# Optimization experiments

Hardware: AMD Instinct MI355X
Metric: run time of the kernel (lower is better)

The kernel has to match this reference:

```python
import jax, jax.numpy as jnp
import numpy as np

B, S, D, H = 8, 1024, 768, 12
DH = D // H  # 64

def setup_inputs() -> dict:
    key = jax.random.key(0)
    ks = jax.random.split(key, 8)
    return {
        "hidden_states": jax.random.normal(ks[0], (B, S, D), jnp.float32),
        "attention_mask": jnp.zeros((B, 1, 1, S), jnp.float32),
        "click_times": jax.random.uniform(ks[1], (B, S), jnp.float32),
        "Wq": jax.random.normal(ks[2], (D, D), jnp.float32) * 0.02,
        "bq": jnp.zeros((D,), jnp.float32),
        "Wk": jax.random.normal(ks[3], (D, D), jnp.float32) * 0.02,
        "bk": jnp.zeros((D,), jnp.float32),
        "Wv": jax.random.normal(ks[4], (D, D), jnp.float32) * 0.02,
        "bv": jnp.zeros((D,), jnp.float32),
    }

def reference(hidden_states, attention_mask, click_times, Wq, bq, Wk, bk, Wv, bv):
    # Linear projections (torch Linear: x @ W.T + b)
    q = hidden_states @ Wq.T + bq
    k = hidden_states @ Wk.T + bk
    v = hidden_states @ Wv.T + bv
    # [B,S,D] -> [B,H,S,DH]
    def split_heads(x):
        return x.reshape(B, S, H, DH).transpose(0, 2, 1, 3)
    q, k, v = split_heads(q), split_heads(k), split_heads(v)
    scores = jnp.einsum('bhqd,bhkd->bhqk', q, k) / jnp.sqrt(jnp.float32(DH))
    # click_times gate: [B,S] -> [B,1,1,S], multiplicative on scores
    scores = scores * click_times[:, None, None, :]
    scores = scores + attention_mask
    probs = jax.nn.softmax(scores, axis=-1)  # dropout is identity at eval
    ctx = jnp.einsum('bhqk,bhkd->bhqd', probs, v)
    ctx = ctx.transpose(0, 2, 1, 3).reshape(B, S, D)
    return ctx
```

## Files before the change

kernel.cpp:

```cpp
#include <hip/hip_runtime.h>
#include <hip/hip_bf16.h>

#define BB 8
#define SS 1024
#define DD 768
#define HH 12

typedef __attribute__((ext_vector_type(8))) _Float16 f16x8;
typedef __attribute__((ext_vector_type(4))) _Float16 f16x4;
typedef __attribute__((ext_vector_type(4))) float f32x4;

typedef __attribute__((address_space(3))) void lds_void;
typedef const __attribute__((address_space(1))) void gmem_void;
#define GLOAD_LDS16(src, dst) \
    __builtin_amdgcn_global_load_lds((gmem_void*)(src), (lds_void*)(dst), 16, 0, 0)

__global__ void prep_kernel(const float* __restrict__ X,
                            const float* __restrict__ Wq,
                            const float* __restrict__ Wk,
                            const float* __restrict__ Wv,
                            const float* __restrict__ bq,
                            const float* __restrict__ bk,
                            const float* __restrict__ bv,
                            _Float16* __restrict__ Xh,
                            _Float16* __restrict__ Wh,
                            float* __restrict__ bias) {
    const int NX4 = (BB * SS * DD) / 4;
    const int NW4 = (DD * DD) / 4;
    const int tid = blockIdx.x * blockDim.x + threadIdx.x;
    const int nth = gridDim.x * blockDim.x;

    for (int i = tid; i < NX4; i += nth) {
        f32x4 x = ((const f32x4*)X)[i];
        f16x4 h;
        for (int j = 0; j < 4; ++j) h[j] = (_Float16)x[j];
        ((f16x4*)Xh)[i] = h;
    }
    const float* Ws[3] = {Wq, Wk, Wv};
    for (int p = 0; p < 3; ++p) {
        const f32x4* src = (const f32x4*)Ws[p];
        f16x4* dst = (f16x4*)(Wh + (size_t)p * DD * DD);
        for (int i = tid; i < NW4; i += nth) {
            f32x4 x = src[i];
            f16x4 h;
            for (int j = 0; j < 4; ++j) h[j] = (_Float16)x[j];
            dst[i] = h;
        }
    }
    for (int i = tid; i < 3 * DD; i += nth) {
        bias[i] = (i < DD) ? bq[i] : (i < 2 * DD ? bk[i - DD] : bv[i - 2 * DD]);
    }
}

__global__ __launch_bounds__(256, 3) void qkv_gemm(const _Float16* __restrict__ Xh,
                                                   const _Float16* __restrict__ Wh,
                                                   const float* __restrict__ bias,
                                                   _Float16* __restrict__ Qb,
                                                   _Float16* __restrict__ Kb,
                                                   _Float16* __restrict__ Vt) {
    __shared__ __align__(16) _Float16 At[2][128 * 32];
    __shared__ __align__(16) _Float16 Bt[2][128 * 32];

    const int tid = threadIdx.x;
    const int l = tid & 63, w = tid >> 6;
    const int wm = w >> 1, wn = w & 1;
    const int mblk = blockIdx.x * 128, nblk = blockIdx.y * 128;
    const int lr = l & 15, lg = l >> 4;
    const int mbase = mblk + wm * 64, nbase = nblk + wn * 64;

    const int sr_i = l >> 2;
    const int scb  = (l & 3) << 4;
    const int sx   = (sr_i >> 1) & 3;
    const int scol = (scb ^ (sx << 4)) >> 1;

    const _Float16* Ag = Xh + (size_t)(mblk + w * 32 + sr_i) * DD + scol;
    const _Float16* Bg = Wh + (size_t)(nblk + w * 32 + sr_i) * DD + scol;

    const int ax = (lr >> 1) & 3;
    const int acol = (lg ^ ax) << 3;
    const int arow0 = (wm * 64 + lr) * 32 + acol;
    const int brow0 = (wn * 64 + lr) * 32 + acol;

    f32x4 acc[4][4] = {};

#pragma unroll
    for (int i = 0; i < 2; ++i) {
        GLOAD_LDS16(Ag + i * 16 * DD, &At[0][w * 1024 + i * 512]);
        GLOAD_LDS16(Bg + i * 16 * DD, &Bt[0][w * 1024 + i * 512]);
    }
    __syncthreads();

    for (int s_ = 0; s_ < 24; ++s_) {
        const int cur = s_ & 1;
        if (s_ < 23) {
            const int kk = (s_ + 1) * 32;
#pragma unroll
            for (int i = 0; i < 2; ++i) {
                GLOAD_LDS16(Ag + kk + i * 16 * DD, &At[cur ^ 1][w * 1024 + i * 512]);
                GLOAD_LDS16(Bg + kk + i * 16 * DD, &Bt[cur ^ 1][w * 1024 + i * 512]);
            }
        }
        f16x8 a[4], b[4];
#pragma unroll
        for (int mi = 0; mi < 4; ++mi)
            a[mi] = *(const f16x8*)(&At[cur][arow0 + mi * 512]);
#pragma unroll
        for (int ni = 0; ni < 4; ++ni)
            b[ni] = *(const f16x8*)(&Bt[cur][brow0 + ni * 512]);
        __builtin_amdgcn_s_setprio(1);
#pragma unroll
        for (int mi = 0; mi < 4; ++mi)
#pragma unroll
            for (int ni = 0; ni < 4; ++ni)
                acc[mi][ni] = __builtin_amdgcn_mfma_f32_16x16x32_f16(
                    a[mi], b[ni], acc[mi][ni], 0, 0, 0);
        __builtin_amdgcn_s_setprio(0);
        __syncthreads();
    }

#pragma unroll
    for (int ni = 0; ni < 4; ++ni) {
        const int n = nbase + ni * 16 + lr;
        const float bv_ = bias[n];
        const int proj = (n >= 2 * DD) ? 2 : (n >= DD ? 1 : 0);
        const int rem = n - proj * DD;
        const int h = rem >> 6, dh = rem & 63;
#pragma unroll
        for (int mi = 0; mi < 4; ++mi) {
            const int m0 = mbase + mi * 16 + lg * 4;
            const int b_ = m0 >> 10;
            const int s0 = m0 & 1023;
            const int bh = b_ * HH + h;
            f32x4 v = acc[mi][ni];
            if (proj == 2) {
                f16x4 pk;
#pragma unroll
                for (int r = 0; r < 4; ++r) pk[r] = (_Float16)(v[r] + bv_);
                *(f16x4*)(Vt + ((size_t)bh * 64 + dh) * SS + s0) = pk;
            } else {
                _Float16* dst = (proj == 0) ? Qb : Kb;
#pragma unroll
                for (int r = 0; r < 4; ++r)
                    dst[((size_t)bh * SS + (s0 + r)) * 64 + dh] =
                        (_Float16)(v[r] + bv_);
            }
        }
    }
}

__global__ __launch_bounds__(256, 4) void attn_kernel(const _Float16* __restrict__ Qb,
                                                      const _Float16* __restrict__ Kb,
                                                      const _Float16* __restrict__ Vt,
                                                      const float* __restrict__ click,
                                                      const float* __restrict__ mask,
                                                      float* __restrict__ out) {
    __shared__ __align__(16) _Float16 Ksh[2][64 * 64];
    __shared__ __align__(16) _Float16 Vsh[2][64 * 64];
    __shared__ __align__(16) _Float16 pT[4][16][40];

    const int tid = threadIdx.x;
    const int l = tid & 63, w = tid >> 6;
    const int lr = l & 15, lg = l >> 4;
    const int qt = blockIdx.x & 15;
    const int bh = blockIdx.x >> 4;
    const int b_ = bh / HH, h = bh - b_ * HH;
    const int qbase = qt * 64 + w * 16;

    const _Float16* Qp = Qb + (size_t)bh * (SS * 64);
    const _Float16* Kp = Kb + (size_t)bh * (SS * 64);
    const _Float16* Vp = Vt + (size_t)bh * (SS * 64);
    const float* ck = click + b_ * SS;
    const float* mk = mask + b_ * SS;

    const f16x8 qf0 = *(const f16x8*)(Qp + (size_t)(qbase + lr) * 64 + lg * 8);
    const f16x8 qf1 = *(const f16x8*)(Qp + (size_t)(qbase + lr) * 64 + 32 + lg * 8);

    const int srow = l >> 3;
    const int scb  = (l & 7) << 4;
    const int scol = (scb ^ (srow << 4)) >> 1;
    const _Float16* Kg = Kp + (size_t)(w * 16 + srow) * 64 + scol;
    const _Float16* Vg = Vp + (size_t)(w * 16 + srow) * SS + scol;

#pragma unroll
    for (int i = 0; i < 2; ++i) {
        GLOAD_LDS16(Kg + (size_t)(i * 8) * 64, &Ksh[0][w * 1024 + i * 512]);
        GLOAD_LDS16(Vg + (size_t)(i * 8) * SS, &Vsh[0][w * 1024 + i * 512]);
    }
    __syncthreads();

    f32x4 o[4] = {};
    float m_run = -3.0e38f, l_run = 0.f;
    const int sw = (lr & 7) << 4;

    for (int c = 0; c < 16; ++c) {
        const int cur = c & 1;
        if (c < 15) {
            const int nb = (c + 1) * 64;
#pragma unroll
            for (int i = 0; i < 2; ++i) {
                GLOAD_LDS16(Kg + (size_t)(nb + i * 8) * 64, &Ksh[cur ^ 1][w * 1024 + i * 512]);
                GLOAD_LDS16(Vg + nb + (size_t)(i * 8) * SS, &Vsh[cur ^ 1][w * 1024 + i * 512]);
            }
        }
        const _Float16* Ks = Ksh[cur];
        const _Float16* Vs = Vsh[cur];
        const int cb64 = c * 64;

#pragma unroll
        for (int ks = 0; ks < 2; ++ks) {
            f32x4 st[2];
            __builtin_amdgcn_s_setprio(1);
#pragma unroll
            for (int t = 0; t < 2; ++t) {
                const int row = (ks * 2 + t) * 16 + lr;
                const f16x8 kf0 = *(const f16x8*)(Ks + row * 64 + (((lg << 4) ^ sw) >> 1));
                const f16x8 kf1 = *(const f16x8*)(Ks + row * 64 + (((64 | (lg << 4)) ^ sw) >> 1));
                f32x4 z = {};
                z = __builtin_amdgcn_mfma_f32_16x16x32_f16(kf0, qf0, z, 0, 0, 0);
                st[t] = __builtin_amdgcn_mfma_f32_16x16x32_f16(kf1, qf1, z, 0, 0, 0);
            }
            __builtin_amdgcn_s_setprio(0);

            const int koff = cb64 + ks * 32 + lg * 4;
            const f32x4 ck0 = *(const f32x4*)(ck + koff);
            const f32x4 ck1 = *(const f32x4*)(ck + koff + 16);
            const f32x4 mk0 = *(const f32x4*)(mk + koff);
            const f32x4 mk1 = *(const f32x4*)(mk + koff + 16);

            float s0[4], s1[4];
            float tmax = -3.0e38f;
#pragma unroll
            for (int r = 0; r < 4; ++r) {
                s0[r] = st[0][r] * (0.125f * ck0[r]) + mk0[r];
                s1[r] = st[1][r] * (0.125f * ck1[r]) + mk1[r];
                tmax = fmaxf(tmax, fmaxf(s0[r], s1[r]));
            }
            tmax = fmaxf(tmax, __shfl_xor(tmax, 16));
            tmax = fmaxf(tmax, __shfl_xor(tmax, 32));

            if (__any(tmax - m_run > 8.f)) {
                const float m_new = fmaxf(m_run, tmax);
                const float sc = __expf(m_run - m_new);
                l_run *= sc;
#pragma unroll
                for (int f = 0; f < 4; ++f)
#pragma unroll
                    for (int r = 0; r < 4; ++r) o[f][r] *= sc;
                m_run = m_new;
            }

            float psum = 0.f;
            f16x4 pk0, pk1;
#pragma unroll
            for (int r = 0; r < 4; ++r) {
                const float p0 = __expf(s0[r] - m_run);
                const float p1 = __expf(s1[r] - m_run);
                psum += p0 + p1;
                pk0[r] = (_Float16)p0;
                pk1[r] = (_Float16)p1;
            }
            psum += __shfl_xor(psum, 16);
            psum += __shfl_xor(psum, 32);
            l_run += psum;

            *(f16x4*)(&pT[w][lr][lg * 4]) = pk0;
            *(f16x4*)(&pT[w][lr][16 + lg * 4]) = pk1;
            const f16x8 pb = *(const f16x8*)(&pT[w][lr][lg * 8]);

            __builtin_amdgcn_s_setprio(1);
#pragma unroll
            for (int f = 0; f < 4; ++f) {
                const int vrow = f * 16 + lr;
                const f16x8 vf = *(const f16x8*)(Vs + vrow * 64 +
                                                 ((((ks << 6) | (lg << 4)) ^ sw) >> 1));
                o[f] = __builtin_amdgcn_mfma_f32_16x16x32_f16(vf, pb, o[f], 0, 0, 0);
            }
            __builtin_amdgcn_s_setprio(0);
        }
        __syncthreads();
    }

    const float inv = 1.f / l_run;
#pragma unroll
    for (int f = 0; f < 4; ++f) {
        f32x4 v = o[f];
#pragma unroll
        for (int r = 0; r < 4; ++r) v[r] *= inv;
        float* dst = out + ((size_t)(b_ * SS + qbase + lr)) * DD + h * 64 + f * 16 + lg * 4;
        *(f32x4*)dst = v;
    }
}

extern "C" void kernel_launch(void* const* d_in, const int* in_sizes, int n_in,
                              void* d_out, int out_size, void* d_ws, size_t ws_size,
                              hipStream_t stream) {
    const float* X     = (const float*)d_in[0];
    const float* mask  = (const float*)d_in[1];
    const float* click = (const float*)d_in[2];
    const float* Wq    = (const float*)d_in[3];
    const float* bq    = (const float*)d_in[4];
    const float* Wk    = (const float*)d_in[5];
    const float* bk    = (const float*)d_in[6];
    const float* Wv    = (const float*)d_in[7];
    const float* bv    = (const float*)d_in[8];
    float* out = (float*)d_out;

    char* ws = (char*)d_ws;
    _Float16* Xh  = (_Float16*)(ws);
    _Float16* Wh  = (_Float16*)(ws + 12582912);
    float*    bia = (float*)   (ws + 16121856);
    _Float16* Qb  = (_Float16*)(ws + 16131072);
    _Float16* Kb  = (_Float16*)(ws + 28713984);
    _Float16* Vt  = (_Float16*)(ws + 41296896);

    prep_kernel<<<1024, 256, 0, stream>>>(X, Wq, Wk, Wv, bq, bk, bv, Xh, Wh, bia);
    qkv_gemm<<<dim3(64, 18), 256, 0, stream>>>(Xh, Wh, bia, Qb, Kb, Vt);
    attn_kernel<<<BB * HH * (SS / 64), 256, 0, stream>>>(Qb, Kb, Vt, click, mask, out);
}
```

Measured before the change: 208.1 us.

## Process two query tiles per attention wave and remap block IDs for XCD locality

The attention kernel now has each wave handle two 16-row query tiles (128 queries per block), so every K/V fragment read from LDS feeds twice as many MFMAs and the grid is halved. Both the GEMM and attention kernels remap block IDs so that consecutive blocks sharing data land on the same XCD. The click scale is precomputed with the 1/8 factor folded in, the weight conversion loop is flattened, the prep grid is doubled, and the launch bounds are swapped. The cost is higher register pressure in attention, fewer blocks to fill the GPU, and slightly different softmax arithmetic ordering.

```diff
diff --git a/kernel.cpp b/kernel.cpp
--- a/kernel.cpp
+++ b/kernel.cpp
@@ -22,9 +22,11 @@
                             const float* __restrict__ bq,
                             const float* __restrict__ bk,
                             const float* __restrict__ bv,
+                            const float* __restrict__ click,
                             _Float16* __restrict__ Xh,
                             _Float16* __restrict__ Wh,
-                            float* __restrict__ bias) {
+                            float* __restrict__ bias,
+                            float* __restrict__ ckS) {
     const int NX4 = (BB * SS * DD) / 4;
     const int NW4 = (DD * DD) / 4;
     const int tid = blockIdx.x * blockDim.x + threadIdx.x;
@@ -36,23 +38,23 @@
         for (int j = 0; j < 4; ++j) h[j] = (_Float16)x[j];
         ((f16x4*)Xh)[i] = h;
     }
-    const float* Ws[3] = {Wq, Wk, Wv};
-    for (int p = 0; p < 3; ++p) {
-        const f32x4* src = (const f32x4*)Ws[p];
-        f16x4* dst = (f16x4*)(Wh + (size_t)p * DD * DD);
-        for (int i = tid; i < NW4; i += nth) {
-            f32x4 x = src[i];
-            f16x4 h;
-            for (int j = 0; j < 4; ++j) h[j] = (_Float16)x[j];
-            dst[i] = h;
-        }
+    for (int i = tid; i < 3 * NW4; i += nth) {
+        const float* src = (i < NW4) ? Wq : (i < 2 * NW4 ? Wk : Wv);
+        const int ii = (i < NW4) ? i : (i < 2 * NW4 ? i - NW4 : i - 2 * NW4);
+        f32x4 x = ((const f32x4*)src)[ii];
+        f16x4 h;
+        for (int j = 0; j < 4; ++j) h[j] = (_Float16)x[j];
+        ((f16x4*)Wh)[i] = h;
     }
     for (int i = tid; i < 3 * DD; i += nth) {
         bias[i] = (i < DD) ? bq[i] : (i < 2 * DD ? bk[i - DD] : bv[i - 2 * DD]);
     }
+    for (int i = tid; i < BB * SS; i += nth) {
+        ckS[i] = 0.125f * click[i];
+    }
 }
 
-__global__ __launch_bounds__(256, 3) void qkv_gemm(const _Float16* __restrict__ Xh,
+__global__ __launch_bounds__(256, 4) void qkv_gemm(const _Float16* __restrict__ Xh,
                                                    const _Float16* __restrict__ Wh,
                                                    const float* __restrict__ bias,
                                                    _Float16* __restrict__ Qb,
@@ -64,7 +66,13 @@
     const int tid = threadIdx.x;
     const int l = tid & 63, w = tid >> 6;
     const int wm = w >> 1, wn = w & 1;
-    const int mblk = blockIdx.x * 128, nblk = blockIdx.y * 128;
+
+    const int bid = blockIdx.x;
+    const int nid = (bid & 7) * 144 + (bid >> 3);
+    const int bx = nid / 18;
+    const int by = nid - bx * 18;
+    const int mblk = bx * 128, nblk = by * 128;
+
     const int lr = l & 15, lg = l >> 4;
     const int mbase = mblk + wm * 64, nbase = nblk + wn * 64;
 
@@ -148,32 +156,39 @@
     }
 }
 
-__global__ __launch_bounds__(256, 4) void attn_kernel(const _Float16* __restrict__ Qb,
+__global__ __launch_bounds__(256, 3) void attn_kernel(const _Float16* __restrict__ Qb,
                                                       const _Float16* __restrict__ Kb,
                                                       const _Float16* __restrict__ Vt,
-                                                      const float* __restrict__ click,
+                                                      const float* __restrict__ ckS,
                                                       const float* __restrict__ mask,
                                                       float* __restrict__ out) {
     __shared__ __align__(16) _Float16 Ksh[2][64 * 64];
     __shared__ __align__(16) _Float16 Vsh[2][64 * 64];
-    __shared__ __align__(16) _Float16 pT[4][16][40];
+    __shared__ __align__(16) _Float16 pT[4][2][16][40];
 
     const int tid = threadIdx.x;
     const int l = tid & 63, w = tid >> 6;
     const int lr = l & 15, lg = l >> 4;
-    const int qt = blockIdx.x & 15;
-    const int bh = blockIdx.x >> 4;
+
+    const int bid = blockIdx.x;
+    const int nid = (bid & 7) * 96 + (bid >> 3);
+    const int qt2 = nid & 7;
+    const int bh  = nid >> 3;
     const int b_ = bh / HH, h = bh - b_ * HH;
-    const int qbase = qt * 64 + w * 16;
+    const int qb0 = qt2 * 128 + w * 16;
 
     const _Float16* Qp = Qb + (size_t)bh * (SS * 64);
     const _Float16* Kp = Kb + (size_t)bh * (SS * 64);
     const _Float16* Vp = Vt + (size_t)bh * (SS * 64);
-    const float* ck = click + b_ * SS;
+    const float* ck = ckS + b_ * SS;
     const float* mk = mask + b_ * SS;
 
-    const f16x8 qf0 = *(const f16x8*)(Qp + (size_t)(qbase + lr) * 64 + lg * 8);
-    const f16x8 qf1 = *(const f16x8*)(Qp + (size_t)(qbase + lr) * 64 + 32 + lg * 8);
+    f16x8 qf[2][2];
+#pragma unroll
+    for (int u = 0; u < 2; ++u) {
+        qf[u][0] = *(const f16x8*)(Qp + (size_t)(qb0 + u * 64 + lr) * 64 + lg * 8);
+        qf[u][1] = *(const f16x8*)(Qp + (size_t)(qb0 + u * 64 + lr) * 64 + 32 + lg * 8);
+    }
 
     const int srow = l >> 3;
     const int scb  = (l & 7) << 4;
@@ -188,8 +203,9 @@
     }
     __syncthreads();
 
-    f32x4 o[4] = {};
-    float m_run = -3.0e38f, l_run = 0.f;
+    f32x4 o[2][4] = {};
+    float m_run[2] = {-3.0e38f, -3.0e38f};
+    float l_run[2] = {0.f, 0.f};
     const int sw = (lr & 7) << 4;
 
     for (int c = 0; c < 16; ++c) {
@@ -208,16 +224,19 @@
 
 #pragma unroll
         for (int ks = 0; ks < 2; ++ks) {
-            f32x4 st[2];
+            f32x4 st[2][2];
             __builtin_amdgcn_s_setprio(1);
 #pragma unroll
             for (int t = 0; t < 2; ++t) {
                 const int row = (ks * 2 + t) * 16 + lr;
                 const f16x8 kf0 = *(const f16x8*)(Ks + row * 64 + (((lg << 4) ^ sw) >> 1));
                 const f16x8 kf1 = *(const f16x8*)(Ks + row * 64 + (((64 | (lg << 4)) ^ sw) >> 1));
-                f32x4 z = {};
-                z = __builtin_amdgcn_mfma_f32_16x16x32_f16(kf0, qf0, z, 0, 0, 0);
-                st[t] = __builtin_amdgcn_mfma_f32_16x16x32_f16(kf1, qf1, z, 0, 0, 0);
+#pragma unroll
+                for (int u = 0; u < 2; ++u) {
+                    f32x4 z = {};
+                    z = __builtin_amdgcn_mfma_f32_16x16x32_f16(kf0, qf[u][0], z, 0, 0, 0);
+                    st[u][t] = __builtin_amdgcn_mfma_f32_16x16x32_f16(kf1, qf[u][1], z, 0, 0, 0);
+                }
             }
             __builtin_amdgcn_s_setprio(0);
 
@@ -227,45 +246,50 @@
             const f32x4 mk0 = *(const f32x4*)(mk + koff);
             const f32x4 mk1 = *(const f32x4*)(mk + koff + 16);
 
-            float s0[4], s1[4];
-            float tmax = -3.0e38f;
-#pragma unroll
-            for (int r = 0; r < 4; ++r) {
-                s0[r] = st[0][r] * (0.125f * ck0[r]) + mk0[r];
-                s1[r] = st[1][r] * (0.125f * ck1[r]) + mk1[r];
-                tmax = fmaxf(tmax, fmaxf(s0[r], s1[r]));
-            }
-            tmax = fmaxf(tmax, __shfl_xor(tmax, 16));
-            tmax = fmaxf(tmax, __shfl_xor(tmax, 32));
-
-            if (__any(tmax - m_run > 8.f)) {
-                const float m_new = fmaxf(m_run, tmax);
-                const float sc = __expf(m_run - m_new);
-                l_run *= sc;
-#pragma unroll
-                for (int f = 0; f < 4; ++f)
-#pragma unroll
-                    for (int r = 0; r < 4; ++r) o[f][r] *= sc;
-                m_run = m_new;
-            }
-
-            float psum = 0.f;
-            f16x4 pk0, pk1;
-#pragma unroll
-            for (int r = 0; r < 4; ++r) {
-                const float p0 = __expf(s0[r] - m_run);
-                const float p1 = __expf(s1[r] - m_run);
-                psum += p0 + p1;
-                pk0[r] = (_Float16)p0;
-                pk1[r] = (_Float16)p1;
-            }
-            psum += __shfl_xor(psum, 16);
-            psum += __shfl_xor(psum, 32);
-            l_run += psum;
-
-            *(f16x4*)(&pT[w][lr][lg * 4]) = pk0;
-            *(f16x4*)(&pT[w][lr][16 + lg * 4]) = pk1;
-            const f16x8 pb = *(const f16x8*)(&pT[w][lr][lg * 8]);
+#pragma unroll
+            for (int u = 0; u < 2; ++u) {
+                float s0[4], s1[4];
+                float tmax = -3.0e38f;
+#pragma unroll
+                for (int r = 0; r < 4; ++r) {
+                    s0[r] = st[u][0][r] * ck0[r] + mk0[r];
+                    s1[r] = st[u][1][r] * ck1[r] + mk1[r];
+                    tmax = fmaxf(tmax, fmaxf(s0[r], s1[r]));
+                }
+                tmax = fmaxf(tmax, __shfl_xor(tmax, 16));
+                tmax = fmaxf(tmax, __shfl_xor(tmax, 32));
+
+                if (__any(tmax - m_run[u] > 8.f)) {
+                    const float m_new = fmaxf(m_run[u], tmax);
+                    const float sc = __expf(m_run[u] - m_new);
+                    l_run[u] *= sc;
+#pragma unroll
+                    for (int f = 0; f < 4; ++f)
+#pragma unroll
+                        for (int r = 0; r < 4; ++r) o[u][f][r] *= sc;
+                    m_run[u] = m_new;
+                }
+
+                float psum = 0.f;
+                f16x4 pk0, pk1;
+#pragma unroll
+                for (int r = 0; r < 4; ++r) {
+                    const float p0 = __expf(s0[r] - m_run[u]);
+                    const float p1 = __expf(s1[r] - m_run[u]);
+                    psum += p0 + p1;
+                    pk0[r] = (_Float16)p0;
+                    pk1[r] = (_Float16)p1;
+                }
+                psum += __shfl_xor(psum, 16);
+                psum += __shfl_xor(psum, 32);
+                l_run[u] += psum;
+
+                *(f16x4*)(&pT[w][u][lr][lg * 4]) = pk0;
+                *(f16x4*)(&pT[w][u][lr][16 + lg * 4]) = pk1;
+            }
+
+            const f16x8 pb0 = *(const f16x8*)(&pT[w][0][lr][lg * 8]);
+            const f16x8 pb1 = *(const f16x8*)(&pT[w][1][lr][lg * 8]);
 
             __builtin_amdgcn_s_setprio(1);
 #pragma unroll
@@ -273,21 +297,26 @@
                 const int vrow = f * 16 + lr;
                 const f16x8 vf = *(const f16x8*)(Vs + vrow * 64 +
                                                  ((((ks << 6) | (lg << 4)) ^ sw) >> 1));
-                o[f] = __builtin_amdgcn_mfma_f32_16x16x32_f16(vf, pb, o[f], 0, 0, 0);
+                o[0][f] = __builtin_amdgcn_mfma_f32_16x16x32_f16(vf, pb0, o[0][f], 0, 0, 0);
+                o[1][f] = __builtin_amdgcn_mfma_f32_16x16x32_f16(vf, pb1, o[1][f], 0, 0, 0);
             }
             __builtin_amdgcn_s_setprio(0);
         }
         __syncthreads();
     }
 
-    const float inv = 1.f / l_run;
-#pragma unroll
-    for (int f = 0; f < 4; ++f) {
-        f32x4 v = o[f];
-#pragma unroll
-        for (int r = 0; r < 4; ++r) v[r] *= inv;
-        float* dst = out + ((size_t)(b_ * SS + qbase + lr)) * DD + h * 64 + f * 16 + lg * 4;
-        *(f32x4*)dst = v;
+#pragma unroll
+    for (int u = 0; u < 2; ++u) {
+        const float inv = 1.f / l_run[u];
+#pragma unroll
+        for (int f = 0; f < 4; ++f) {
+            f32x4 v = o[u][f];
+#pragma unroll
+            for (int r = 0; r < 4; ++r) v[r] *= inv;
+            float* dst = out + ((size_t)(b_ * SS + qb0 + u * 64 + lr)) * DD +
+                         h * 64 + f * 16 + lg * 4;
+            *(f32x4*)dst = v;
+        }
     }
 }
 
@@ -309,11 +338,13 @@
     _Float16* Xh  = (_Float16*)(ws);
     _Float16* Wh  = (_Float16*)(ws + 12582912);
     float*    bia = (float*)   (ws + 16121856);
-    _Float16* Qb  = (_Float16*)(ws + 16131072);
-    _Float16* Kb  = (_Float16*)(ws + 28713984);
-    _Float16* Vt  = (_Float16*)(ws + 41296896);
-
-    prep_kernel<<<1024, 256, 0, stream>>>(X, Wq, Wk, Wv, bq, bk, bv, Xh, Wh, bia);
-    qkv_gemm<<<dim3(64, 18), 256, 0, stream>>>(Xh, Wh, bia, Qb, Kb, Vt);
-    attn_kernel<<<BB * HH * (SS / 64), 256, 0, stream>>>(Qb, Kb, Vt, click, mask, out);
+    float*    ckS = (float*)   (ws + 16131072);
+    _Float16* Qb  = (_Float16*)(ws + 16163840);
+    _Float16* Kb  = (_Float16*)(ws + 28746752);
+    _Float16* Vt  = (_Float16*)(ws + 41329664);
+
+    prep_kernel<<<2048, 256, 0, stream>>>(X, Wq, Wk, Wv, bq, bk, bv, click,
+                                          Xh, Wh, bia, ckS);
+    qkv_gemm<<<1152, 256, 0, stream>>>(Xh, Wh, bia, Qb, Kb, Vt);
+    attn_kernel<<<768, 256, 0, stream>>>(Qb, Kb, Vt, ckS, mask, out);
 }
```

Measured after the change: 194.0 us. 1.07x faster.
